# Optimization experiments

Hardware: AMD Instinct MI355X
Metric: run time of the kernel (lower is better)

The kernel has to match this reference:

```python
import jax, jax.numpy as jnp
import numpy as np

B, Q, K, D = 32, 1024, 1024, 128

def setup_inputs() -> dict:
    key = jax.random.key(0)
    kq, kk, kv, kl = jax.random.split(key, 4)
    return {
        "queries": jax.random.normal(kq, (B, Q, D), dtype=jnp.float32),
        "keys": jax.random.normal(kk, (B, K, D), dtype=jnp.float32),
        "values": jax.random.normal(kv, (B, K, D), dtype=jnp.float32),
        "valid_length": jax.random.randint(kl, (B,), 1, K + 1),
    }

def reference(queries, keys, values, valid_length):
    d = queries.shape[-1]
    # scores: [B, Q, K]
    scores = jnp.einsum("bqd,bkd->bqk", queries, keys) / jnp.sqrt(jnp.float32(d))
    # length mask: position k is valid iff k < valid_length[b]
    mask = jnp.arange(keys.shape[1])[None, None, :] < valid_length[:, None, None]
    scores = jnp.where(mask, scores, jnp.float32(-1e9))
    attn = jax.nn.softmax(scores, axis=-1)
    # dropout module is identity in eval / p=0
    return jnp.einsum("bqk,bkv->bqv", attn, values)
```

## Files before the change

### kernel.cpp

```cpp
#include <hip/hip_runtime.h>
#include <hip/hip_bf16.h>
#include <stdint.h>

#define B_    32
#define QLEN  1024
#define KSEQ  1024
#define DIM   128
#define NKT   (KSEQ / 64)
#define SCALE 0.08838834764831845f

typedef __attribute__((ext_vector_type(8))) short  short8;
typedef __attribute__((ext_vector_type(4))) float  floatx4;
typedef unsigned int u32;

__device__ __forceinline__ u32 f2bf(float x) {
  union { float f; u32 u; } v; v.f = x;
  return (v.u + 0x7FFF + ((v.u >> 16) & 1)) >> 16;
}
__device__ __forceinline__ u32 pack2(float lo, float hi) {
  return f2bf(lo) | (f2bf(hi) << 16);
}

__device__ __forceinline__ void barrier_full() {
  asm volatile("s_waitcnt vmcnt(0) lgkmcnt(0)" ::: "memory");
  __syncthreads();
}

__global__ __launch_bounds__(256) void prep_kernel(const float* __restrict__ Kg,
                                                   const float* __restrict__ Vg,
                                                   const int* __restrict__ vlen,
                                                   uint4* __restrict__ Ksw,
                                                   uint4* __restrict__ Vsw,
                                                   int2* __restrict__ task) {
  __shared__ __align__(16) u32 Vu[64 * 65];
  __shared__ int sidx[32];
  const int kt = blockIdx.x, b = blockIdx.y, t = threadIdx.x;
  const bool tableblk = (blockIdx.z == 0) && (kt == 0) && (b == 0);

  if (tableblk && t < 64) {
    const int bb = t & 31;
    const int ntb = (vlen[bb] + 63) >> 6;
    int rank = 0;
#pragma unroll
    for (int j = 0; j < 32; j++) {
      const int ntj = __shfl(ntb, j);
      rank += (ntj > ntb) | ((ntj == ntb) & (j < bb));
    }
    if (t < 32) sidx[rank] = bb;
  }

  if (kt * 64 < vlen[b]) {
    if (blockIdx.z == 0) {
      const float* src = Kg + ((size_t)b * KSEQ + kt * 64) * DIM;
      uint4* dst = Ksw + ((size_t)b * NKT + kt) * 1024;
#pragma unroll
      for (int it = 0; it < 4; it++) {
        const int f = it * 256 + t, r = f >> 4, c = f & 15;
        floatx4 f0 = *(const floatx4*)(src + r * DIM + c * 8);
        floatx4 f1 = *(const floatx4*)(src + r * DIM + c * 8 + 4);
        uint4 o;
        o.x = pack2(f0[0], f0[1]); o.y = pack2(f0[2], f0[3]);
        o.z = pack2(f1[0], f1[1]); o.w = pack2(f1[2], f1[3]);
        dst[r * 16 + (c ^ (r & 15))] = o;
      }
    } else {
      const float* src = Vg + ((size_t)b * KSEQ + kt * 64) * DIM;
#pragma unroll
      for (int it = 0; it < 8; it++) {
        const int k = it * 8 + (t >> 5), c = t & 31;
        const floatx4 f = *(const floatx4*)(src + (size_t)k * DIM + c * 4);
        const int s = (k >> 3) & 4;
        Vu[k * 65 + ((2 * c) ^ s)]     = pack2(f[0], f[1]);
        Vu[k * 65 + ((2 * c + 1) ^ s)] = pack2(f[2], f[3]);
      }
      __syncthreads();
      uint4* dst = Vsw + ((size_t)b * NKT + kt) * 1024;
#pragma unroll
      for (int it = 0; it < 4; it++) {
        const int id = it * 256 + t;
        const int kc = id & 7, d = (id >> 3) & 127;
        const int col = (d >> 1) ^ (kc & 4);
        u32 r[8];
#pragma unroll
        for (int j = 0; j < 8; j++) r[j] = Vu[(kc * 8 + j) * 65 + col];
        const u32 sel = (d & 1) ? 0x07060302u : 0x05040100u;
        uint4 o;
        o.x = __builtin_amdgcn_perm(r[1], r[0], sel);
        o.y = __builtin_amdgcn_perm(r[3], r[2], sel);
        o.z = __builtin_amdgcn_perm(r[5], r[4], sel);
        o.w = __builtin_amdgcn_perm(r[7], r[6], sel);
        dst[d * 8 + (kc ^ (d & 7))] = o;
      }
    }
  }

  if (tableblk) {
    __syncthreads();
    for (int l = t; l < 512; l += 256) {
      const int x = l & 7, j = l >> 3;
      int rank, q;
      if (j < 32) { rank = (j & 1) ? x + 8  : x;      q = j >> 1; }
      else        { rank = (j & 1) ? x + 16 : x + 24; q = (j - 32) >> 1; }
      task[l] = make_int2(sidx[rank], q << 6);
    }
  }
}

typedef const __attribute__((address_space(1))) u32* as1p;
typedef __attribute__((address_space(3))) u32* as3p;
__device__ __forceinline__ void gl_lds16(const void* g, void* l) {
  __builtin_amdgcn_global_load_lds((as1p)g, (as3p)l, 16, 0, 0);
}

__global__ __launch_bounds__(256, 2) void attn_kernel(
    const float* __restrict__ Qg, const uint4* __restrict__ Ksw,
    const uint4* __restrict__ Vsw, const int* __restrict__ vlen,
    const int2* __restrict__ task, float* __restrict__ Og) {
  __shared__ __align__(16) short Kbuf[2][64 * 128];
  __shared__ __align__(16) short Vbuf[2][128 * 64];
  __shared__ __align__(16) short Pl[4][16][72];

  const int2 tq = task[blockIdx.x];
  const int b = tq.x, q0 = tq.y;
  const int t = threadIdx.x, wave = t >> 6, lane = t & 63;
  const int quad = lane >> 4, m = lane & 15;
  const int L  = vlen[b];
  const int nt = (L + 63) >> 6;

  const char* Kt = (const char*)(Ksw + (size_t)b * NKT * 1024);
  const char* Vt = (const char*)(Vsw + (size_t)b * NKT * 1024);

  short8 aq[4];
  {
    const float* qrow = Qg + ((size_t)b * QLEN + q0 + wave * 16 + m) * DIM;
#pragma unroll
    for (int c = 0; c < 4; c++) {
      floatx4 f0 = *(const floatx4*)(qrow + c * 32 + quad * 8);
      floatx4 f1 = *(const floatx4*)(qrow + c * 32 + quad * 8 + 4);
      short8 a;
      a[0] = (short)f2bf(f0[0]); a[1] = (short)f2bf(f0[1]);
      a[2] = (short)f2bf(f0[2]); a[3] = (short)f2bf(f0[3]);
      a[4] = (short)f2bf(f1[0]); a[5] = (short)f2bf(f1[1]);
      a[6] = (short)f2bf(f1[2]); a[7] = (short)f2bf(f1[3]);
      aq[c] = a;
    }
  }

  float lrow[4];
  floatx4 oacc[8];
#pragma unroll
  for (int r = 0; r < 4; r++) lrow[r] = 0.0f;
#pragma unroll
  for (int d = 0; d < 8; d++) oacc[d] = (floatx4){0.f, 0.f, 0.f, 0.f};

#define ISSUE_K(tk, bb)                                                        \
  {                                                                            \
    const char* g_ = Kt + (size_t)(tk) * 16384 + wave * 4096 + lane * 16;      \
    _Pragma("unroll") for (int i_ = 0; i_ < 4; i_++)                           \
        gl_lds16(g_ + i_ * 1024, (char*)Kbuf[bb] + wave * 4096 + i_ * 1024);   \
  }
#define ISSUE_V(tk, bb)                                                        \
  {                                                                            \
    const char* g_ = Vt + (size_t)(tk) * 16384 + wave * 4096 + lane * 16;      \
    _Pragma("unroll") for (int i_ = 0; i_ < 4; i_++)                           \
        gl_lds16(g_ + i_ * 1024, (char*)Vbuf[bb] + wave * 4096 + i_ * 1024);   \
  }

  ISSUE_K(0, 0);
  ISSUE_V(0, 0);

  for (int tk = 0; tk < nt; tk++) {
    const int k0 = tk * 64;
    barrier_full();
    if (tk + 1 < nt) {
      ISSUE_K(tk + 1, (tk + 1) & 1);
      ISSUE_V(tk + 1, (tk + 1) & 1);
    }
    const short* Kb_ = Kbuf[tk & 1];
    const short* Vb_ = Vbuf[tk & 1];

    floatx4 sa[4];
#pragma unroll
    for (int s = 0; s < 4; s++) sa[s] = (floatx4){0.f, 0.f, 0.f, 0.f};
    __builtin_amdgcn_s_setprio(1);
#pragma unroll
    for (int s = 0; s < 4; s++) {
#pragma unroll
      for (int c = 0; c < 4; c++) {
        const short8 bk = *(const short8*)(Kb_ + (s * 16 + m) * 128 +
                                           (((c * 4 + quad) ^ m) & 15) * 8);
        sa[s] = __builtin_amdgcn_mfma_f32_16x16x32_bf16(aq[c], bk, sa[s], 0, 0, 0);
      }
    }
    __builtin_amdgcn_s_setprio(0);

    float p[4][4];
    if (k0 + 64 <= L) {
#pragma unroll
      for (int s = 0; s < 4; s++)
#pragma unroll
        for (int r = 0; r < 4; r++)
          p[s][r] = __expf(fminf(sa[s][r] * SCALE, 30.0f));
    } else {
      const bool vv[4] = {(k0 + m) < L, (k0 + 16 + m) < L,
                          (k0 + 32 + m) < L, (k0 + 48 + m) < L};
#pragma unroll
      for (int s = 0; s < 4; s++)
#pragma unroll
        for (int r = 0; r < 4; r++)
          p[s][r] = vv[s] ? __expf(fminf(sa[s][r] * SCALE, 30.0f)) : 0.0f;
    }
#pragma unroll
    for (int r = 0; r < 4; r++)
      lrow[r] += (p[0][r] + p[1][r]) + (p[2][r] + p[3][r]);

#pragma unroll
    for (int s = 0; s < 4; s++) {
#pragma unroll
      for (int r = 0; r < 4; r++)
        Pl[wave][quad * 4 + r][s * 16 + m] = (short)f2bf(p[s][r]);
    }
    asm volatile("s_waitcnt lgkmcnt(0)" ::: "memory");
    const short8 pa0 = *(const short8*)&Pl[wave][m][quad * 8];
    const short8 pa1 = *(const short8*)&Pl[wave][m][32 + quad * 8];

    __builtin_amdgcn_s_setprio(1);
#pragma unroll
    for (int d = 0; d < 8; d++) {
      const int row = d * 16 + m;
      const short8 bv0 = *(const short8*)(Vb_ + row * 64 + ((quad ^ (m & 7)) & 7) * 8);
      const short8 bv1 = *(const short8*)(Vb_ + row * 64 + (((quad + 4) ^ (m & 7)) & 7) * 8);
      oacc[d] = __builtin_amdgcn_mfma_f32_16x16x32_bf16(pa0, bv0, oacc[d], 0, 0, 0);
      oacc[d] = __builtin_amdgcn_mfma_f32_16x16x32_bf16(pa1, bv1, oacc[d], 0, 0, 0);
    }
    __builtin_amdgcn_s_setprio(0);
  }

#pragma unroll
  for (int off = 1; off < 16; off <<= 1) {
#pragma unroll
    for (int r = 0; r < 4; r++) lrow[r] += __shfl_xor(lrow[r], off);
  }
  float inv[4];
#pragma unroll
  for (int r = 0; r < 4; r++) inv[r] = 1.0f / lrow[r];
  float* orow = Og + ((size_t)b * QLEN + q0 + wave * 16) * DIM;
#pragma unroll
  for (int d = 0; d < 8; d++) {
#pragma unroll
    for (int r = 0; r < 4; r++)
      orow[(size_t)(quad * 4 + r) * DIM + d * 16 + m] = oacc[d][r] * inv[r];
  }
#undef ISSUE_K
#undef ISSUE_V
}

extern "C" void kernel_launch(void* const* d_in, const int* in_sizes, int n_in,
                              void* d_out, int out_size, void* d_ws, size_t ws_size,
                              hipStream_t stream) {
  const float* Qg = (const float*)d_in[0];
  const float* Kg = (const float*)d_in[1];
  const float* Vg = (const float*)d_in[2];
  const int*  vln = (const int*)d_in[3];
  uint4* Ksw = (uint4*)d_ws;
  uint4* Vsw = (uint4*)((char*)d_ws + (size_t)B_ * NKT * 16384);
  int2*  Tsk = (int2*)((char*)d_ws + 2 * (size_t)B_ * NKT * 16384);

  prep_kernel<<<dim3(NKT, B_, 2), 256, 0, stream>>>(Kg, Vg, vln, Ksw, Vsw, Tsk);
  attn_kernel<<<dim3(512), 256, 0, stream>>>(Qg, Ksw, Vsw, vln, Tsk,
                                             (float*)d_out);
}
```

Measured before the change: 118.5 us.

## Switch attention to 32x32x16 MFMA with transposed scores and register-only P

Rewrites the attention inner loop to use 32x32x16 bf16 MFMA instead of 16x16x32. Scores are computed transposed (K as the A operand, Q as B), so the softmax probabilities can be packed with v_cvt_pk_bf16_f32 and rearranged with v_permlane32_swap into the PV operand layout. This removes the LDS round-trip through the Pl buffer and its wait. Each block now has 2 waves of 32 query rows instead of 4 waves of 16, so per-wave register pressure and load issue per wave go up, and occupancy may fall.

```diff
diff --git a/kernel.cpp b/kernel.cpp
--- a/kernel.cpp
+++ b/kernel.cpp
@@ -9,8 +9,9 @@
 #define NKT   (KSEQ / 64)
 #define SCALE 0.08838834764831845f
 
-typedef __attribute__((ext_vector_type(8))) short  short8;
-typedef __attribute__((ext_vector_type(4))) float  floatx4;
+typedef __attribute__((ext_vector_type(8)))  short short8;
+typedef __attribute__((ext_vector_type(4)))  float floatx4;
+typedef __attribute__((ext_vector_type(16))) float floatx16;
 typedef unsigned int u32;
 
 __device__ __forceinline__ u32 f2bf(float x) {
@@ -20,6 +21,15 @@
 __device__ __forceinline__ u32 pack2(float lo, float hi) {
   return f2bf(lo) | (f2bf(hi) << 16);
 }
+__device__ __forceinline__ u32 cvtpk(float lo, float hi) {
+  u32 d;
+  asm("v_cvt_pk_bf16_f32 %0, %1, %2" : "=v"(d) : "v"(lo), "v"(hi));
+  return d;
+}
+__device__ __forceinline__ void swap32(u32& a, u32& b) {
+  asm volatile("v_permlane32_swap_b32 %0, %1" : "+v"(a), "+v"(b));
+}
+typedef union { uint4 u; short8 s; } U8;
 
 __device__ __forceinline__ void barrier_full() {
   asm volatile("s_waitcnt vmcnt(0) lgkmcnt(0)" ::: "memory");
@@ -112,62 +122,82 @@
   __builtin_amdgcn_global_load_lds((as1p)g, (as3p)l, 16, 0, 0);
 }
 
-__global__ __launch_bounds__(256, 2) void attn_kernel(
+__global__ __launch_bounds__(128, 1) void attn_kernel(
     const float* __restrict__ Qg, const uint4* __restrict__ Ksw,
     const uint4* __restrict__ Vsw, const int* __restrict__ vlen,
     const int2* __restrict__ task, float* __restrict__ Og) {
   __shared__ __align__(16) short Kbuf[2][64 * 128];
   __shared__ __align__(16) short Vbuf[2][128 * 64];
-  __shared__ __align__(16) short Pl[4][16][72];
 
   const int2 tq = task[blockIdx.x];
   const int b = tq.x, q0 = tq.y;
   const int t = threadIdx.x, wave = t >> 6, lane = t & 63;
-  const int quad = lane >> 4, m = lane & 15;
+  const int l31 = lane & 31, hi = lane >> 5, m15 = l31 & 15, m7 = l31 & 7;
   const int L  = vlen[b];
   const int nt = (L + 63) >> 6;
 
   const char* Kt = (const char*)(Ksw + (size_t)b * NKT * 1024);
   const char* Vt = (const char*)(Vsw + (size_t)b * NKT * 1024);
 
-  short8 aq[4];
+  short8 qb[8];
   {
-    const float* qrow = Qg + ((size_t)b * QLEN + q0 + wave * 16 + m) * DIM;
-#pragma unroll
-    for (int c = 0; c < 4; c++) {
-      floatx4 f0 = *(const floatx4*)(qrow + c * 32 + quad * 8);
-      floatx4 f1 = *(const floatx4*)(qrow + c * 32 + quad * 8 + 4);
+    const float* qrow = Qg + ((size_t)b * QLEN + q0 + wave * 32 + l31) * DIM;
+#pragma unroll
+    for (int c = 0; c < 8; c++) {
+      floatx4 f0 = *(const floatx4*)(qrow + c * 16 + hi * 8);
+      floatx4 f1 = *(const floatx4*)(qrow + c * 16 + hi * 8 + 4);
       short8 a;
       a[0] = (short)f2bf(f0[0]); a[1] = (short)f2bf(f0[1]);
       a[2] = (short)f2bf(f0[2]); a[3] = (short)f2bf(f0[3]);
       a[4] = (short)f2bf(f1[0]); a[5] = (short)f2bf(f1[1]);
       a[6] = (short)f2bf(f1[2]); a[7] = (short)f2bf(f1[3]);
-      aq[c] = a;
-    }
-  }
-
-  float lrow[4];
-  floatx4 oacc[8];
-#pragma unroll
-  for (int r = 0; r < 4; r++) lrow[r] = 0.0f;
-#pragma unroll
-  for (int d = 0; d < 8; d++) oacc[d] = (floatx4){0.f, 0.f, 0.f, 0.f};
+      qb[c] = a;
+    }
+  }
+
+  float lrow = 0.0f;
+  floatx16 oacc[4];
+#pragma unroll
+  for (int dt = 0; dt < 4; dt++)
+#pragma unroll
+    for (int i = 0; i < 16; i++) oacc[dt][i] = 0.0f;
 
 #define ISSUE_K(tk, bb)                                                        \
   {                                                                            \
-    const char* g_ = Kt + (size_t)(tk) * 16384 + wave * 4096 + lane * 16;      \
-    _Pragma("unroll") for (int i_ = 0; i_ < 4; i_++)                           \
-        gl_lds16(g_ + i_ * 1024, (char*)Kbuf[bb] + wave * 4096 + i_ * 1024);   \
+    const char* g_ = Kt + (size_t)(tk) * 16384 + wave * 8192 + lane * 16;      \
+    _Pragma("unroll") for (int i_ = 0; i_ < 8; i_++)                           \
+        gl_lds16(g_ + i_ * 1024, (char*)Kbuf[bb] + wave * 8192 + i_ * 1024);   \
   }
 #define ISSUE_V(tk, bb)                                                        \
   {                                                                            \
-    const char* g_ = Vt + (size_t)(tk) * 16384 + wave * 4096 + lane * 16;      \
-    _Pragma("unroll") for (int i_ = 0; i_ < 4; i_++)                           \
-        gl_lds16(g_ + i_ * 1024, (char*)Vbuf[bb] + wave * 4096 + i_ * 1024);   \
+    const char* g_ = Vt + (size_t)(tk) * 16384 + wave * 8192 + lane * 16;      \
+    _Pragma("unroll") for (int i_ = 0; i_ < 8; i_++)                           \
+        gl_lds16(g_ + i_ * 1024, (char*)Vbuf[bb] + wave * 8192 + i_ * 1024);   \
   }
 
   ISSUE_K(0, 0);
   ISSUE_V(0, 0);
+
+#define PV_TILE(SV, KC0, KC1)                                                  \
+  {                                                                            \
+    u32 u0 = cvtpk(SV[0], SV[1]),   u1 = cvtpk(SV[2], SV[3]);                  \
+    u32 u2 = cvtpk(SV[4], SV[5]),   u3 = cvtpk(SV[6], SV[7]);                  \
+    swap32(u0, u2); swap32(u1, u3);                                            \
+    u32 w0 = cvtpk(SV[8], SV[9]),   w1 = cvtpk(SV[10], SV[11]);                \
+    u32 w2 = cvtpk(SV[12], SV[13]), w3 = cvtpk(SV[14], SV[15]);                \
+    swap32(w0, w2); swap32(w1, w3);                                            \
+    U8 pu0; pu0.u.x = u0; pu0.u.y = u1; pu0.u.z = u2; pu0.u.w = u3;            \
+    U8 pu1; pu1.u.x = w0; pu1.u.y = w1; pu1.u.z = w2; pu1.u.w = w3;            \
+    __builtin_amdgcn_s_setprio(1);                                             \
+    _Pragma("unroll") for (int dt = 0; dt < 4; dt++) {                         \
+      const short* vr_ = Vb_ + (dt * 32 + l31) * 64;                           \
+      const short8 b0_ = *(const short8*)(vr_ + ((KC0) ^ m7) * 8);             \
+      oacc[dt] = __builtin_amdgcn_mfma_f32_32x32x16_bf16(pu0.s, b0_, oacc[dt], 0, 0, 0); \
+      const short8 b1_ = *(const short8*)(vr_ + ((KC1) ^ m7) * 8);             \
+      oacc[dt] = __builtin_amdgcn_mfma_f32_32x32x16_bf16(pu1.s, b1_, oacc[dt], 0, 0, 0); \
+    }                                                                          \
+    __builtin_amdgcn_s_setprio(0);                                             \
+  }
 
   for (int tk = 0; tk < nt; tk++) {
     const int k0 = tk * 64;
@@ -179,80 +209,64 @@
     const short* Kb_ = Kbuf[tk & 1];
     const short* Vb_ = Vbuf[tk & 1];
 
-    floatx4 sa[4];
-#pragma unroll
-    for (int s = 0; s < 4; s++) sa[s] = (floatx4){0.f, 0.f, 0.f, 0.f};
-    __builtin_amdgcn_s_setprio(1);
-#pragma unroll
-    for (int s = 0; s < 4; s++) {
-#pragma unroll
-      for (int c = 0; c < 4; c++) {
-        const short8 bk = *(const short8*)(Kb_ + (s * 16 + m) * 128 +
-                                           (((c * 4 + quad) ^ m) & 15) * 8);
-        sa[s] = __builtin_amdgcn_mfma_f32_16x16x32_bf16(aq[c], bk, sa[s], 0, 0, 0);
-      }
-    }
-    __builtin_amdgcn_s_setprio(0);
-
-    float p[4][4];
+    floatx16 s0, s1;
+#pragma unroll
+    for (int i = 0; i < 16; i++) { s0[i] = 0.0f; s1[i] = 0.0f; }
+    {
+      const short* kr0 = Kb_ + l31 * 128;
+      const short* kr1 = Kb_ + (32 + l31) * 128;
+      __builtin_amdgcn_s_setprio(1);
+#pragma unroll
+      for (int c = 0; c < 8; c++) {
+        const int cp = ((2 * c + hi) ^ m15) * 8;
+        const short8 ka0 = *(const short8*)(kr0 + cp);
+        const short8 ka1 = *(const short8*)(kr1 + cp);
+        s0 = __builtin_amdgcn_mfma_f32_32x32x16_bf16(ka0, qb[c], s0, 0, 0, 0);
+        s1 = __builtin_amdgcn_mfma_f32_32x32x16_bf16(ka1, qb[c], s1, 0, 0, 0);
+      }
+      __builtin_amdgcn_s_setprio(0);
+    }
+
     if (k0 + 64 <= L) {
 #pragma unroll
-      for (int s = 0; s < 4; s++)
-#pragma unroll
-        for (int r = 0; r < 4; r++)
-          p[s][r] = __expf(fminf(sa[s][r] * SCALE, 30.0f));
+      for (int r = 0; r < 16; r++) {
+        s0[r] = __expf(fminf(s0[r] * SCALE, 30.0f));
+        s1[r] = __expf(fminf(s1[r] * SCALE, 30.0f));
+        lrow += s0[r] + s1[r];
+      }
     } else {
-      const bool vv[4] = {(k0 + m) < L, (k0 + 16 + m) < L,
-                          (k0 + 32 + m) < L, (k0 + 48 + m) < L};
-#pragma unroll
-      for (int s = 0; s < 4; s++)
-#pragma unroll
-        for (int r = 0; r < 4; r++)
-          p[s][r] = vv[s] ? __expf(fminf(sa[s][r] * SCALE, 30.0f)) : 0.0f;
-    }
-#pragma unroll
-    for (int r = 0; r < 4; r++)
-      lrow[r] += (p[0][r] + p[1][r]) + (p[2][r] + p[3][r]);
-
-#pragma unroll
-    for (int s = 0; s < 4; s++) {
-#pragma unroll
-      for (int r = 0; r < 4; r++)
-        Pl[wave][quad * 4 + r][s * 16 + m] = (short)f2bf(p[s][r]);
-    }
-    asm volatile("s_waitcnt lgkmcnt(0)" ::: "memory");
-    const short8 pa0 = *(const short8*)&Pl[wave][m][quad * 8];
-    const short8 pa1 = *(const short8*)&Pl[wave][m][32 + quad * 8];
-
-    __builtin_amdgcn_s_setprio(1);
-#pragma unroll
-    for (int d = 0; d < 8; d++) {
-      const int row = d * 16 + m;
-      const short8 bv0 = *(const short8*)(Vb_ + row * 64 + ((quad ^ (m & 7)) & 7) * 8);
-      const short8 bv1 = *(const short8*)(Vb_ + row * 64 + (((quad + 4) ^ (m & 7)) & 7) * 8);
-      oacc[d] = __builtin_amdgcn_mfma_f32_16x16x32_bf16(pa0, bv0, oacc[d], 0, 0, 0);
-      oacc[d] = __builtin_amdgcn_mfma_f32_16x16x32_bf16(pa1, bv1, oacc[d], 0, 0, 0);
-    }
-    __builtin_amdgcn_s_setprio(0);
-  }
-
-#pragma unroll
-  for (int off = 1; off < 16; off <<= 1) {
-#pragma unroll
-    for (int r = 0; r < 4; r++) lrow[r] += __shfl_xor(lrow[r], off);
-  }
-  float inv[4];
-#pragma unroll
-  for (int r = 0; r < 4; r++) inv[r] = 1.0f / lrow[r];
-  float* orow = Og + ((size_t)b * QLEN + q0 + wave * 16) * DIM;
-#pragma unroll
-  for (int d = 0; d < 8; d++) {
-#pragma unroll
-    for (int r = 0; r < 4; r++)
-      orow[(size_t)(quad * 4 + r) * DIM + d * 16 + m] = oacc[d][r] * inv[r];
+#pragma unroll
+      for (int r = 0; r < 16; r++) {
+        const int ck = (r & 3) + 8 * (r >> 2) + 4 * hi;
+        const float a0 = (k0 + ck < L)      ? __expf(fminf(s0[r] * SCALE, 30.0f)) : 0.0f;
+        const float a1 = (k0 + 32 + ck < L) ? __expf(fminf(s1[r] * SCALE, 30.0f)) : 0.0f;
+        s0[r] = a0; s1[r] = a1;
+        lrow += a0 + a1;
+      }
+    }
+
+    PV_TILE(s0, 0 + hi, 2 + hi);
+    PV_TILE(s1, 4 + hi, 6 + hi);
+  }
+
+  lrow += __shfl_xor(lrow, 32);
+  const float inv_ = 1.0f / lrow;
+  float iv[16];
+#pragma unroll
+  for (int r = 0; r < 16; r++)
+    iv[r] = __shfl(inv_, (r & 3) + 8 * (r >> 2) + 4 * hi);
+  float* obase = Og + ((size_t)b * QLEN + q0 + wave * 32) * DIM + l31;
+#pragma unroll
+  for (int dt = 0; dt < 4; dt++) {
+#pragma unroll
+    for (int r = 0; r < 16; r++) {
+      const int rq = (r & 3) + 8 * (r >> 2) + 4 * hi;
+      obase[(size_t)rq * DIM + dt * 32] = oacc[dt][r] * iv[r];
+    }
   }
 #undef ISSUE_K
 #undef ISSUE_V
+#undef PV_TILE
 }
 
 extern "C" void kernel_launch(void* const* d_in, const int* in_sizes, int n_in,
@@ -267,6 +281,6 @@
   int2*  Tsk = (int2*)((char*)d_ws + 2 * (size_t)B_ * NKT * 16384);
 
   prep_kernel<<<dim3(NKT, B_, 2), 256, 0, stream>>>(Kg, Vg, vln, Ksw, Vsw, Tsk);
-  attn_kernel<<<dim3(512), 256, 0, stream>>>(Qg, Ksw, Vsw, vln, Tsk,
+  attn_kernel<<<dim3(512), 128, 0, stream>>>(Qg, Ksw, Vsw, vln, Tsk,
                                              (float*)d_out);
 }
```

After: 124.4 us. 1.05x slower.
